# Kernel tuning notes

Measured on AMD Instinct MI355X. Metric: run time of the kernel, lower is better.

The kernel has to match this reference:

```python
import jax, jax.numpy as jnp
import numpy as np

N_SAMPLES = 256
D_IN = 512
D_HID = 1024


def setup_inputs() -> dict:
    key = jax.random.key(0)
    k1, k2, k3, k4, k5, k6 = jax.random.split(key, 6)
    x1 = jax.random.normal(k1, (N_SAMPLES, D_IN), dtype=jnp.float32)
    x2 = jax.random.normal(k2, (N_SAMPLES, D_IN), dtype=jnp.float32)
    # MLP params with fan-in scaling (realistic init)
    W1 = jax.random.normal(k3, (D_IN, D_HID), dtype=jnp.float32) / np.sqrt(D_IN)
    b1 = jax.random.normal(k4, (D_HID,), dtype=jnp.float32) * 0.01
    W2 = jax.random.normal(k5, (D_HID, 1), dtype=jnp.float32) / np.sqrt(D_HID)
    b2 = jax.random.normal(k6, (1,), dtype=jnp.float32) * 0.01
    return {"x1": x1, "x2": x2, "W1": W1, "b1": b1, "W2": W2, "b2": b2}


def _per_sample_jacobian(params, x):
    """Per-sample grads of scalar network output w.r.t. params, flattened.

    params: (W1, b1, W2, b2); x: [n, d_in]. Returns J: [n, P].
    """
    def f_single(p, xi):  # xi: [d_in] -> scalar (matches squeeze(-1) in torch)
        W1, b1, W2, b2 = p
        h = jax.nn.relu(xi @ W1 + b1)          # [d_hid]
        return (h @ W2 + b2)[0]                # scalar

    grads = jax.vmap(jax.grad(f_single), in_axes=(None, 0))(params, x)
    n = x.shape[0]
    return jnp.concatenate(
        [g.reshape(n, -1) for g in jax.tree_util.tree_leaves(grads)], axis=1
    )


def reference(x1, x2, W1, b1, W2, b2):
    params = (W1, b1, W2, b2)
    J1 = _per_sample_jacobian(params, x1)  # [n, P]
    J2 = _per_sample_jacobian(params, x2)  # [n, P]
    # Empirical NTK: K[i,j] = <grad_i, grad_j> -- single fused GEMM instead of
    # the original O(n^2) autograd.grad loop.
    return J1 @ J2.T                       # [n, n]
```

## Files before the change

### kernel.cpp

```cpp
#include <hip/hip_runtime.h>
#include <hip/hip_bf16.h>

#define NS   256
#define DIN  512
#define DHID 1024

typedef __attribute__((ext_vector_type(8))) short bf16x8;
typedef __attribute__((ext_vector_type(4))) float f32x4;

static __device__ __forceinline__ short f2bf(float f) {
    return __builtin_bit_cast(short, __float2bfloat16(f));
}

static __device__ __forceinline__ bf16x8 cvt8(f32x4 a, f32x4 b) {
    bf16x8 r;
    r[0] = f2bf(a[0]); r[1] = f2bf(a[1]); r[2] = f2bf(a[2]); r[3] = f2bf(a[3]);
    r[4] = f2bf(b[0]); r[5] = f2bf(b[1]); r[6] = f2bf(b[2]); r[7] = f2bf(b[3]);
    return r;
}

__global__ __launch_bounds__(256, 3) void ntk_k1(
    const float* __restrict__ x1, const float* __restrict__ x2,
    const float* __restrict__ W1, const float* __restrict__ b1,
    const float* __restrict__ w2,
    short* __restrict__ Hb, short* __restrict__ Gb,
    float* __restrict__ Cws)
{
    const int tid = threadIdx.x;
    const int l   = tid & 63;
    const int w   = tid >> 6;
    const int lr  = l & 15;
    const int kg  = l >> 4;
    const int b   = blockIdx.x;

    if (b < 512) {
        const int m0  = (b >> 4) * 16;
        const int col = (b & 15) * 64 + w * 16 + lr;
        const float* X = (m0 < NS) ? (x1 + (size_t)m0 * DIN)
                                   : (x2 + (size_t)(m0 - NS) * DIN);
        const float* ap = X + lr * DIN;
        const float* bp = W1 + (size_t)(kg * 8) * DHID + col;

        f32x4 acc = {0.f, 0.f, 0.f, 0.f};
        #pragma unroll 4
        for (int t = 0; t < 16; ++t) {
            const int k = t * 32 + kg * 8;
            bf16x8 a = cvt8(*(const f32x4*)(ap + k), *(const f32x4*)(ap + k + 4));
            f32x4 b0v, b1v;
            #pragma unroll
            for (int i = 0; i < 4; ++i) b0v[i] = bp[(size_t)(t * 32 + i) * DHID];
            #pragma unroll
            for (int i = 0; i < 4; ++i) b1v[i] = bp[(size_t)(t * 32 + 4 + i) * DHID];
            bf16x8 bf = cvt8(b0v, b1v);
            acc = __builtin_amdgcn_mfma_f32_16x16x32_bf16(a, bf, acc, 0, 0, 0);
        }

        const float bbv = b1[col], wwv = w2[col];
        #pragma unroll
        for (int r = 0; r < 4; ++r) {
            const int row = m0 + kg * 4 + r;
            float z = acc[r] + bbv;
            Hb[row * DHID + col] = f2bf(z > 0.f ? z   : 0.f);
            Gb[row * DHID + col] = f2bf(z > 0.f ? wwv : 0.f);
        }
    } else {
        __shared__ f32x4 red[4][64];
        const int bb = b - 512;
        const int bi = (bb >> 4) * 16;
        const int bj = (bb & 15) * 16;

        const float* ar = x1 + (bi + lr) * DIN + kg * 8;
        const float* br = x2 + (bj + lr) * DIN + kg * 8;
        f32x4 ac = {0.f, 0.f, 0.f, 0.f};
        #pragma unroll
        for (int t = 0; t < 4; ++t) {
            const int k = (w + t * 4) * 32;
            bf16x8 a  = cvt8(*(const f32x4*)(ar + k), *(const f32x4*)(ar + k + 4));
            bf16x8 bv = cvt8(*(const f32x4*)(br + k), *(const f32x4*)(br + k + 4));
            ac = __builtin_amdgcn_mfma_f32_16x16x32_bf16(a, bv, ac, 0, 0, 0);
        }
        red[w][l] = ac;
        __syncthreads();
        if (w == 0) {
            f32x4 c = red[0][l];
            #pragma unroll
            for (int q = 1; q < 4; ++q) c += red[q][l];
            #pragma unroll
            for (int r = 0; r < 4; ++r)
                Cws[(bi + kg * 4 + r) * NS + (bj + lr)] = c[r];
        }
    }
}

__global__ __launch_bounds__(512) void ntk_k2(
    const short* __restrict__ Hb, const short* __restrict__ Gb,
    const float* __restrict__ Cws, float* __restrict__ out)
{
    const int tid = threadIdx.x;
    const int l   = tid & 63;
    const int w   = tid >> 6;
    const int lr  = l & 15;
    const int kg  = l >> 4;
    const int bi  = (blockIdx.x >> 4) * 16;
    const int bj  = (blockIdx.x & 15) * 16;

    __shared__ f32x4 red[2][8][64];

    f32x4 ag = {0.f,0.f,0.f,0.f}, ah = {0.f,0.f,0.f,0.f};

    const short* ga = Gb + (bi + lr) * DHID + kg * 8;
    const short* gb = Gb + (NS + bj + lr) * DHID + kg * 8;
    const short* ha = Hb + (bi + lr) * DHID + kg * 8;
    const short* hb = Hb + (NS + bj + lr) * DHID + kg * 8;

    #pragma unroll
    for (int t = 0; t < 4; ++t) {
        const int k = (w + t * 8) * 32;
        bf16x8 a  = *(const bf16x8*)(ga + k);
        bf16x8 bv = *(const bf16x8*)(gb + k);
        ag = __builtin_amdgcn_mfma_f32_16x16x32_bf16(a, bv, ag, 0, 0, 0);
        bf16x8 a2 = *(const bf16x8*)(ha + k);
        bf16x8 b2 = *(const bf16x8*)(hb + k);
        ah = __builtin_amdgcn_mfma_f32_16x16x32_bf16(a2, b2, ah, 0, 0, 0);
    }

    red[0][w][l] = ag; red[1][w][l] = ah;
    __syncthreads();
    if (w == 0) {
        f32x4 g = red[0][0][l], h = red[1][0][l];
        #pragma unroll
        for (int q = 1; q < 8; ++q) { g += red[0][q][l]; h += red[1][q][l]; }
        #pragma unroll
        for (int r = 0; r < 4; ++r) {
            const int idx = (bi + kg * 4 + r) * NS + (bj + lr);
            out[idx] = (Cws[idx] + 1.f) * g[r] + h[r] + 1.f;
        }
    }
}

extern "C" void kernel_launch(void* const* d_in, const int* in_sizes, int n_in,
                              void* d_out, int out_size, void* d_ws, size_t ws_size,
                              hipStream_t stream) {
    const float* x1 = (const float*)d_in[0];
    const float* x2 = (const float*)d_in[1];
    const float* W1 = (const float*)d_in[2];
    const float* b1 = (const float*)d_in[3];
    const float* w2 = (const float*)d_in[4];

    short* Hb  = (short*)d_ws;
    short* Gb  = Hb + 2 * NS * DHID;
    float* Cws = (float*)(Gb + 2 * NS * DHID);
    float* out = (float*)d_out;

    ntk_k1<<<768, 256, 0, stream>>>(x1, x2, W1, b1, w2, Hb, Gb, Cws);
    ntk_k2<<<256, 512, 0, stream>>>(Hb, Gb, Cws, out);
}
```

Baseline: 24.43 us.

## Switch first kernel to 32x32x16 MFMA tiles with fewer larger blocks

The first kernel now uses 32x32x16 bf16 MFMA instead of 16x16x32 for both the hidden-layer GEMM and the x1·x2ᵀ Gram part. Each wave computes a 32x32 output tile, which halves redundant global loads and fp32-to-bf16 conversions per output, and the grid shrinks from 768 to 192 blocks. The trade-off is fewer blocks than the chip has compute units and larger per-wave register and shared-memory footprint, which may reduce parallelism and latency hiding. The occupancy hint in launch bounds is dropped.

Measured after the change: 22.92 us. -6.2%, faster.

```diff
diff --git a/kernel.cpp b/kernel.cpp
--- a/kernel.cpp
+++ b/kernel.cpp
@@ -5,8 +5,9 @@
 #define DIN  512
 #define DHID 1024
 
-typedef __attribute__((ext_vector_type(8))) short bf16x8;
-typedef __attribute__((ext_vector_type(4))) float f32x4;
+typedef __attribute__((ext_vector_type(8)))  short bf16x8;
+typedef __attribute__((ext_vector_type(4)))  float f32x4;
+typedef __attribute__((ext_vector_type(16))) float f32x16;
 
 static __device__ __forceinline__ short f2bf(float f) {
     return __builtin_bit_cast(short, __float2bfloat16(f));
@@ -19,7 +20,7 @@
     return r;
 }
 
-__global__ __launch_bounds__(256, 3) void ntk_k1(
+__global__ __launch_bounds__(256) void ntk_k1(
     const float* __restrict__ x1, const float* __restrict__ x2,
     const float* __restrict__ W1, const float* __restrict__ b1,
     const float* __restrict__ w2,
@@ -29,65 +30,68 @@
     const int tid = threadIdx.x;
     const int l   = tid & 63;
     const int w   = tid >> 6;
-    const int lr  = l & 15;
-    const int kg  = l >> 4;
+    const int lc  = l & 31;
+    const int hk  = l >> 5;
     const int b   = blockIdx.x;
 
-    if (b < 512) {
-        const int m0  = (b >> 4) * 16;
-        const int col = (b & 15) * 64 + w * 16 + lr;
-        const float* X = (m0 < NS) ? (x1 + (size_t)m0 * DIN)
-                                   : (x2 + (size_t)(m0 - NS) * DIN);
-        const float* ap = X + lr * DIN;
-        const float* bp = W1 + (size_t)(kg * 8) * DHID + col;
+    __shared__ f32x16 red[4][64];
 
-        f32x4 acc = {0.f, 0.f, 0.f, 0.f};
+    if (b < 128) {
+        const int m0  = (b >> 3) * 32;
+        const int col = (b & 7) * 128 + w * 32 + lc;
+        const float* X  = (m0 < NS) ? (x1 + (size_t)m0 * DIN)
+                                    : (x2 + (size_t)(m0 - NS) * DIN);
+        const float* ap = X + lc * DIN + hk * 8;
+        const float* bp = W1 + (size_t)(hk * 8) * DHID + col;
+
+        f32x16 acc = {};
         #pragma unroll 4
-        for (int t = 0; t < 16; ++t) {
-            const int k = t * 32 + kg * 8;
-            bf16x8 a = cvt8(*(const f32x4*)(ap + k), *(const f32x4*)(ap + k + 4));
+        for (int t = 0; t < 32; ++t) {
+            const int k0 = t * 16;
+            bf16x8 a = cvt8(*(const f32x4*)(ap + k0), *(const f32x4*)(ap + k0 + 4));
             f32x4 b0v, b1v;
             #pragma unroll
-            for (int i = 0; i < 4; ++i) b0v[i] = bp[(size_t)(t * 32 + i) * DHID];
+            for (int i = 0; i < 4; ++i) b0v[i] = bp[(size_t)(k0 + i) * DHID];
             #pragma unroll
-            for (int i = 0; i < 4; ++i) b1v[i] = bp[(size_t)(t * 32 + 4 + i) * DHID];
+            for (int i = 0; i < 4; ++i) b1v[i] = bp[(size_t)(k0 + 4 + i) * DHID];
             bf16x8 bf = cvt8(b0v, b1v);
-            acc = __builtin_amdgcn_mfma_f32_16x16x32_bf16(a, bf, acc, 0, 0, 0);
+            acc = __builtin_amdgcn_mfma_f32_32x32x16_bf16(a, bf, acc, 0, 0, 0);
         }
 
         const float bbv = b1[col], wwv = w2[col];
         #pragma unroll
-        for (int r = 0; r < 4; ++r) {
-            const int row = m0 + kg * 4 + r;
+        for (int r = 0; r < 16; ++r) {
+            const int row = m0 + (r & 3) + 8 * (r >> 2) + 4 * hk;
             float z = acc[r] + bbv;
             Hb[row * DHID + col] = f2bf(z > 0.f ? z   : 0.f);
             Gb[row * DHID + col] = f2bf(z > 0.f ? wwv : 0.f);
         }
     } else {
-        __shared__ f32x4 red[4][64];
-        const int bb = b - 512;
-        const int bi = (bb >> 4) * 16;
-        const int bj = (bb & 15) * 16;
+        const int bb = b - 128;
+        const int bi = (bb >> 3) * 32;
+        const int bj = (bb & 7) * 32;
+        const float* ar = x1 + (bi + lc) * DIN + hk * 8;
+        const float* br = x2 + (bj + lc) * DIN + hk * 8;
 
-        const float* ar = x1 + (bi + lr) * DIN + kg * 8;
-        const float* br = x2 + (bj + lr) * DIN + kg * 8;
-        f32x4 ac = {0.f, 0.f, 0.f, 0.f};
+        f32x16 ac = {};
         #pragma unroll
-        for (int t = 0; t < 4; ++t) {
-            const int k = (w + t * 4) * 32;
-            bf16x8 a  = cvt8(*(const f32x4*)(ar + k), *(const f32x4*)(ar + k + 4));
-            bf16x8 bv = cvt8(*(const f32x4*)(br + k), *(const f32x4*)(br + k + 4));
-            ac = __builtin_amdgcn_mfma_f32_16x16x32_bf16(a, bv, ac, 0, 0, 0);
+        for (int q = 0; q < 8; ++q) {
+            const int k0 = (w + q * 4) * 16;
+            bf16x8 a  = cvt8(*(const f32x4*)(ar + k0), *(const f32x4*)(ar + k0 + 4));
+            bf16x8 bv = cvt8(*(const f32x4*)(br + k0), *(const f32x4*)(br + k0 + 4));
+            ac = __builtin_amdgcn_mfma_f32_32x32x16_bf16(a, bv, ac, 0, 0, 0);
         }
         red[w][l] = ac;
         __syncthreads();
         if (w == 0) {
-            f32x4 c = red[0][l];
+            f32x16 c = red[0][l];
             #pragma unroll
             for (int q = 1; q < 4; ++q) c += red[q][l];
             #pragma unroll
-            for (int r = 0; r < 4; ++r)
-                Cws[(bi + kg * 4 + r) * NS + (bj + lr)] = c[r];
+            for (int r = 0; r < 16; ++r) {
+                const int row = bi + (r & 3) + 8 * (r >> 2) + 4 * hk;
+                Cws[row * NS + (bj + lc)] = c[r];
+            }
         }
     }
 }
@@ -152,6 +156,6 @@
     float* Cws = (float*)(Gb + 2 * NS * DHID);
     float* out = (float*)d_out;
 
-    ntk_k1<<<768, 256, 0, stream>>>(x1, x2, W1, b1, w2, Hb, Gb, Cws);
+    ntk_k1<<<192, 256, 0, stream>>>(x1, x2, W1, b1, w2, Hb, Gb, Cws);
     ntk_k2<<<256, 512, 0, stream>>>(Hb, Gb, Cws, out);
 }
```
